# Kernel tuning notes

Hardware: AMD Instinct MI355X
Metric: run time of the kernel (lower is better)

Reference implementation:

```python
import jax, jax.numpy as jnp
import numpy as np

B, C, H = 16, 512, 32
HID, NB, S, P, SR = 512, 36, 26, 7, 2
SCALE = 32.0
N_LOC, N_LOC_LAB = 12, 8
N_GRP, GRP_SZ, N_GRP_LAB = 4, 6, 16
IN_DIM = P * P * C


def roi_align(feat, coords, scale, pooled, sr):
    # feat: (B,C,H,W); coords: (B,NB,4) normalized xyxy. torchvision roi_align,
    # aligned=False, fixed sampling_ratio=sr (adaptive ratio is data-dependent).
    Bs, Cc, Hh, Ww = feat.shape
    x1 = coords[..., 0] * scale
    y1 = coords[..., 1] * scale
    x2 = coords[..., 2] * scale
    y2 = coords[..., 3] * scale
    rw = jnp.maximum(x2 - x1, 1.0)
    rh = jnp.maximum(y2 - y1, 1.0)
    bw = rw / pooled
    bh = rh / pooled
    # sample offsets within roi, in bin units: (pooled*sr,)
    off = (jnp.arange(pooled)[:, None] + (jnp.arange(sr) + 0.5) / sr).reshape(-1)
    ys = y1[..., None] + off * bh[..., None]  # (B,NB,pooled*sr)
    xs = x1[..., None] + off * bw[..., None]

    def prep(t, size):
        valid = (t > -1.0) & (t < size)
        tc = jnp.clip(t, 0.0, size - 1)
        lo = jnp.floor(tc).astype(jnp.int32)
        hi = jnp.minimum(lo + 1, size - 1)
        frac = tc - lo
        return lo, hi, frac, valid

    y_lo, y_hi, ly, vy = prep(ys, Hh)
    x_lo, x_hi, lx, vx = prep(xs, Ww)
    hy, hx = 1.0 - ly, 1.0 - lx

    featl = feat.transpose(0, 2, 3, 1)  # (B,H,W,C)
    b_idx = jnp.arange(Bs)[:, None, None, None]

    def gather(yi, xi):
        # -> (B,NB,Py,Px,C)
        return featl[b_idx, yi[:, :, :, None], xi[:, :, None, :]]

    def w(a, b):
        return (a[..., :, None] * b[..., None, :])[..., None]

    val = (gather(y_lo, x_lo) * w(hy, hx) + gather(y_lo, x_hi) * w(hy, lx)
           + gather(y_hi, x_lo) * w(ly, hx) + gather(y_hi, x_hi) * w(ly, lx))
    mask = (vy[:, :, :, None] & vx[:, :, None, :])[..., None]
    val = jnp.where(mask, val, 0.0)
    val = val.reshape(Bs, -1, pooled, sr, pooled, sr, Cc).mean(axis=(3, 5))
    return val.transpose(0, 1, 4, 2, 3)  # (B,NB,C,pooled,pooled)


def setup_inputs() -> dict:
    key = jax.random.key(0)
    ks = jax.random.split(key, 10)
    lf = jax.random.normal(ks[0], (B, C, H, H), dtype=jnp.float32)
    xs = jnp.sort(jax.random.uniform(ks[1], (B, S, 2)), axis=-1)
    ys = jnp.sort(jax.random.uniform(ks[2], (B, S, 2)), axis=-1)
    coords = jnp.stack([xs[..., 0], ys[..., 0], xs[..., 1], ys[..., 1]], axis=-1)
    sc = 0.02
    return {
        'local_features': lf,
        'pred_bbox_coords': coords,
        'roi_fc_W': jax.random.normal(ks[3], (HID, IN_DIM), dtype=jnp.float32) * sc,
        'roi_fc_b': jnp.zeros((HID,), jnp.float32),
        'coords_W': jax.random.normal(ks[4], (S, 4, HID), dtype=jnp.float32) * sc,
        'coords_b': jnp.zeros((S, 4), jnp.float32),
        'pres_W': jax.random.normal(ks[5], (S, HID), dtype=jnp.float32) * sc,
        'pres_b': jnp.zeros((S,), jnp.float32),
        'loc_W': jax.random.normal(ks[6], (N_LOC, N_LOC_LAB, HID), dtype=jnp.float32) * sc,
        'loc_b': jnp.zeros((N_LOC, N_LOC_LAB), jnp.float32),
        'grp_W': jax.random.normal(ks[7], (N_GRP, N_GRP_LAB, GRP_SZ * HID), dtype=jnp.float32) * sc,
        'grp_b': jnp.zeros((N_GRP, N_GRP_LAB), jnp.float32),
        'loc_idx': jnp.arange(N_LOC, dtype=jnp.int32),
        'grp_idx': jnp.arange(N_GRP * GRP_SZ, dtype=jnp.int32).reshape(N_GRP, GRP_SZ),
    }


def reference(local_features, pred_bbox_coords, roi_fc_W, roi_fc_b, coords_W,
              coords_b, pres_W, pres_b, loc_W, loc_b, grp_W, grp_b, loc_idx, grp_idx):
    Bs = local_features.shape[0]
    # boxes S..NB default to the full image (0,0,1,1)
    full = jnp.broadcast_to(jnp.array([0.0, 0.0, 1.0, 1.0], jnp.float32), (Bs, NB, 4))
    coords_all = full.at[:, :S].set(pred_bbox_coords)
    roi = roi_align(local_features, coords_all, SCALE, P, SR)  # (B,NB,C,P,P)
    flat = roi.reshape(Bs, NB, IN_DIM)
    feats = jax.nn.relu(jnp.einsum('bnf,hf->bnh', flat, roi_fc_W) + roi_fc_b)
    sup = feats[:, :S]  # (B,S,HID)
    # per-box coord refinement heads
    deltas = jnp.einsum('bsh,soh->bso', sup, coords_W) + coords_b  # (B,S,4)
    w = pred_bbox_coords[..., 2] - pred_bbox_coords[..., 0]
    h = pred_bbox_coords[..., 3] - pred_bbox_coords[..., 1]
    wh = jnp.stack([w, h, w, h], axis=-1)
    refined = pred_bbox_coords + deltas * wh
    presence = jnp.einsum('bsh,sh->bs', sup, pres_W) + pres_b  # (B,S)
    # per-box MLC heads
    loc = jnp.einsum('blh,loh->blo', feats[:, loc_idx], loc_W) + loc_b
    # per-group MLC heads (concat box feats within group along hidden)
    gf = feats[:, grp_idx].reshape(Bs, N_GRP, GRP_SZ * HID)
    grp = jnp.einsum('bgk,gok->bgo', gf, grp_W) + grp_b
    mlc = jnp.concatenate([loc.reshape(Bs, -1), grp.reshape(Bs, -1)], axis=1)
    return refined, presence, mlc
```

## Files before the change

### kernel.cpp

```cpp
#include <hip/hip_runtime.h>

typedef unsigned short u16;
typedef __attribute__((ext_vector_type(8))) short short8;
typedef __attribute__((ext_vector_type(8))) unsigned short ushort8_t;
typedef __attribute__((ext_vector_type(4))) float f32x4;
typedef __attribute__((ext_vector_type(2))) float v2f;

#define BATCH   16
#define CCH     512
#define NBOX    36
#define SS      26
#define INDIM   25088
#define HIDN    512
#define M_ROWS  576
#define KSPLIT  28
#define KITERS  14

__device__ __forceinline__ u16 f2bf(float f) {
  unsigned u = __float_as_uint(f);
  u += 0x7FFF + ((u >> 16) & 1);
  return (u16)(u >> 16);
}
__device__ __forceinline__ float bf2f(u16 h) {
  return __uint_as_float(((unsigned)h) << 16);
}
__device__ __forceinline__ v2f bf2x2(u16 a, u16 b) {
  v2f r;
  r.x = __uint_as_float(((unsigned)a) << 16);
  r.y = __uint_as_float(((unsigned)b) << 16);
  return r;
}

typedef __attribute__((address_space(3))) void* as3_ptr;
typedef const __attribute__((address_space(1))) void* as1_cptr;
__device__ __forceinline__ void gload_lds16(const void* g, void* l) {
  __builtin_amdgcn_global_load_lds((as1_cptr)g, (as3_ptr)l, 16, 0, 0);
}

__global__ __launch_bounds__(256) void k_transpose_lf(const float* __restrict__ in,
                                                      u16* __restrict__ out) {
  __shared__ float t[32][33];
  int b = blockIdx.z, ct = blockIdx.y, pt = blockIdx.x;
  int tx = threadIdx.x, ty = threadIdx.y;
#pragma unroll
  for (int i = 0; i < 4; ++i) {
    int c = ct * 32 + ty + i * 8;
    int p = pt * 32 + tx;
    t[ty + i * 8][tx] = in[((size_t)b * CCH + c) * 1024 + p];
  }
  __syncthreads();
#pragma unroll
  for (int i = 0; i < 4; ++i) {
    int p = pt * 32 + ty + i * 8;
    int c = ct * 32 + tx;
    out[((size_t)b * 1024 + p) * CCH + c] = f2bf(t[tx][ty + i * 8]);
  }
}

__global__ __launch_bounds__(256) void k_convert_w(const float4* __restrict__ in,
                                                   ushort4* __restrict__ out) {
  int i = blockIdx.x * 256 + threadIdx.x;
  float4 v = in[i];
  ushort4 o;
  o.x = f2bf(v.x); o.y = f2bf(v.y); o.z = f2bf(v.z); o.w = f2bf(v.w);
  out[i] = o;
}

__global__ __launch_bounds__(512) void k_roi(const u16* __restrict__ lf_t,
                                             const float* __restrict__ pred,
                                             u16* __restrict__ flat) {
  __shared__ int   s_ylo[14], s_yhi[14], s_xlo[14], s_xhi[14];
  __shared__ float s_wyl[14], s_wyh[14], s_wxl[14], s_wxh[14];
  __shared__ u16   s_out[INDIM];

  int blk = blockIdx.x;
  int b = blk / NBOX, n = blk % NBOX;
  int t = threadIdx.x;

  if (t < 28) {
    bool isY = t < 14;
    int j = isY ? t : t - 14;
    float c0, c1, c2, c3;
    if (n < SS) {
      const float* p = pred + ((size_t)(b * SS + n)) * 4;
      c0 = p[0]; c1 = p[1]; c2 = p[2]; c3 = p[3];
    } else { c0 = 0.f; c1 = 0.f; c2 = 1.f; c3 = 1.f; }
    float lo1 = (isY ? c1 : c0) * 32.f;
    float hi1 = (isY ? c3 : c2) * 32.f;
    float sz = fmaxf(hi1 - lo1, 1.f);
    float bs = sz * (1.f / 7.f);
    float off = (float)(j >> 1) + 0.25f + 0.5f * (float)(j & 1);
    float pos = lo1 + off * bs;
    bool valid = (pos > -1.f) && (pos < 32.f);
    float tc = fminf(fmaxf(pos, 0.f), 31.f);
    int lo = (int)floorf(tc);
    int hi = min(lo + 1, 31);
    float fr = tc - (float)lo;
    float wl = valid ? (1.f - fr) : 0.f;
    float wh = valid ? fr : 0.f;
    if (isY) { s_ylo[j] = lo; s_yhi[j] = hi; s_wyl[j] = wl; s_wyh[j] = wh; }
    else     { s_xlo[j] = lo; s_xhi[j] = hi; s_wxl[j] = wl; s_wxh[j] = wh; }
  }
  __syncthreads();

  int cg = t & 63;
  int pg = t >> 6;
  const u16* base = lf_t + (size_t)b * 1024 * CCH + cg * 8;

  for (int p = pg; p < 49; p += 8) {
    int py = p / 7, px = p % 7;
    v2f a0 = {0.f, 0.f}, a1 = {0.f, 0.f}, a2 = {0.f, 0.f}, a3 = {0.f, 0.f};
#pragma unroll
    for (int sy = 0; sy < 2; ++sy) {
      int jy = 2 * py + sy;
      const u16* rlo = base + s_ylo[jy] * 32 * CCH;
      const u16* rhi = base + s_yhi[jy] * 32 * CCH;
      float wyl = s_wyl[jy], wyh = s_wyh[jy];
#pragma unroll
      for (int sx = 0; sx < 2; ++sx) {
        int jx = 2 * px + sx;
        int xl = s_xlo[jx] * CCH, xh = s_xhi[jx] * CCH;
        v2f wll = {wyl * s_wxl[jx], wyl * s_wxl[jx]};
        v2f wlh = {wyl * s_wxh[jx], wyl * s_wxh[jx]};
        v2f whl = {wyh * s_wxl[jx], wyh * s_wxl[jx]};
        v2f whh = {wyh * s_wxh[jx], wyh * s_wxh[jx]};
        ushort8_t vll = *(const ushort8_t*)(rlo + xl);
        ushort8_t vlh = *(const ushort8_t*)(rlo + xh);
        ushort8_t vhl = *(const ushort8_t*)(rhi + xl);
        ushort8_t vhh = *(const ushort8_t*)(rhi + xh);
        a0 += wll * bf2x2(vll[0], vll[1]) + wlh * bf2x2(vlh[0], vlh[1])
            + whl * bf2x2(vhl[0], vhl[1]) + whh * bf2x2(vhh[0], vhh[1]);
        a1 += wll * bf2x2(vll[2], vll[3]) + wlh * bf2x2(vlh[2], vlh[3])
            + whl * bf2x2(vhl[2], vhl[3]) + whh * bf2x2(vhh[2], vhh[3]);
        a2 += wll * bf2x2(vll[4], vll[5]) + wlh * bf2x2(vlh[4], vlh[5])
            + whl * bf2x2(vhl[4], vhl[5]) + whh * bf2x2(vhh[4], vhh[5]);
        a3 += wll * bf2x2(vll[6], vll[7]) + wlh * bf2x2(vlh[6], vlh[7])
            + whl * bf2x2(vhl[6], vhl[7]) + whh * bf2x2(vhh[6], vhh[7]);
      }
    }
    int c0i = cg * 8;
    s_out[(c0i + 0) * 49 + p] = f2bf(a0.x * 0.25f);
    s_out[(c0i + 1) * 49 + p] = f2bf(a0.y * 0.25f);
    s_out[(c0i + 2) * 49 + p] = f2bf(a1.x * 0.25f);
    s_out[(c0i + 3) * 49 + p] = f2bf(a1.y * 0.25f);
    s_out[(c0i + 4) * 49 + p] = f2bf(a2.x * 0.25f);
    s_out[(c0i + 5) * 49 + p] = f2bf(a2.y * 0.25f);
    s_out[(c0i + 6) * 49 + p] = f2bf(a3.x * 0.25f);
    s_out[(c0i + 7) * 49 + p] = f2bf(a3.y * 0.25f);
  }
  __syncthreads();

  uint4* dst = (uint4*)(flat + (size_t)blk * INDIM);
  const uint4* src = (const uint4*)s_out;
  for (int i = t; i < INDIM / 8; i += 512) dst[i] = src[i];
}

__global__ __launch_bounds__(256) void k_gemm(const u16* __restrict__ flat,
                                              const u16* __restrict__ Wb,
                                              float* __restrict__ partials) {
  __shared__ u16 As[128 * 64];
  __shared__ u16 Bs[64 * 64];

  int tid = threadIdx.x;
  int wave = tid >> 6, lane = tid & 63;
  int wm = wave >> 1, wn = wave & 1;
  int quad = lane >> 4, r = lane & 15;
  int xb = r & 7;

  int tileM0 = blockIdx.y * 128;
  int tileN0 = blockIdx.x * 64;
  int kbase = blockIdx.z * (KITERS * 64);

  f32x4 acc[4][2];
#pragma unroll
  for (int mi = 0; mi < 4; ++mi)
#pragma unroll
    for (int ni = 0; ni < 2; ++ni) acc[mi][ni] = (f32x4){0.f, 0.f, 0.f, 0.f};

  for (int kt = 0; kt < KITERS; ++kt) {
    int k0 = kbase + kt * 64;
#pragma unroll
    for (int t = 0; t < 4; ++t) {
      int chunk = (wave * 4 + t) * 64 + lane;
      int row = chunk >> 3;
      int pcol = chunk & 7;
      int lcol = ((pcol ^ (row & 7)) << 3);
      int grow = min(tileM0 + row, M_ROWS - 1);
      gload_lds16(flat + (size_t)grow * INDIM + k0 + lcol,
                  &As[(wave * 4 + t) * 512]);
    }
#pragma unroll
    for (int t = 0; t < 2; ++t) {
      int chunk = (wave * 2 + t) * 64 + lane;
      int row = chunk >> 3;
      int pcol = chunk & 7;
      int lcol = ((pcol ^ (row & 7)) << 3);
      int nrow = tileN0 + row;
      gload_lds16(Wb + (size_t)nrow * INDIM + k0 + lcol,
                  &Bs[(wave * 2 + t) * 512]);
    }
    __syncthreads();

#pragma unroll
    for (int kk = 0; kk < 64; kk += 32) {
      int k8 = kk >> 3;
      int pc = ((k8 + quad) ^ xb) << 3;
      short8 af[4], bfr[2];
#pragma unroll
      for (int mi = 0; mi < 4; ++mi)
        af[mi] = *(const short8*)&As[(wm * 64 + mi * 16 + r) * 64 + pc];
#pragma unroll
      for (int ni = 0; ni < 2; ++ni)
        bfr[ni] = *(const short8*)&Bs[(wn * 32 + ni * 16 + r) * 64 + pc];
#pragma unroll
      for (int mi = 0; mi < 4; ++mi)
#pragma unroll
        for (int ni = 0; ni < 2; ++ni)
          acc[mi][ni] = __builtin_amdgcn_mfma_f32_16x16x32_bf16(
              af[mi], bfr[ni], acc[mi][ni], 0, 0, 0);
    }
    __syncthreads();
  }

  float* part = partials + (size_t)blockIdx.z * (M_ROWS * HIDN);
#pragma unroll
  for (int mi = 0; mi < 4; ++mi)
#pragma unroll
    for (int ni = 0; ni < 2; ++ni) {
      int row0 = tileM0 + wm * 64 + mi * 16 + quad * 4;
      int col = tileN0 + wn * 32 + ni * 16 + r;
#pragma unroll
      for (int reg = 0; reg < 4; ++reg) {
        int row = row0 + reg;
        if (row < M_ROWS) part[(size_t)row * HIDN + col] = acc[mi][ni][reg];
      }
    }
}

__global__ __launch_bounds__(256) void k_reduce(const float* __restrict__ partials,
                                                const float* __restrict__ bias,
                                                float* __restrict__ feats) {
  int gid = blockIdx.x * 256 + threadIdx.x;
  int h = gid & (HIDN - 1);
  float s = 0.f;
#pragma unroll
  for (int k = 0; k < KSPLIT; ++k) s += partials[(size_t)k * (M_ROWS * HIDN) + gid];
  s += bias[h];
  feats[gid] = fmaxf(s, 0.f);
}

__device__ __forceinline__ float wave_red(float s) {
#pragma unroll
  for (int off = 32; off > 0; off >>= 1) s += __shfl_down(s, off);
  return s;
}

__device__ __forceinline__ float dot512(const float* __restrict__ f,
                                        const float* __restrict__ w, int lane) {
  const float4* f4 = (const float4*)f;
  const float4* w4 = (const float4*)w;
  float4 x0 = f4[lane], y0 = w4[lane];
  float4 x1 = f4[lane + 64], y1 = w4[lane + 64];
  return x0.x * y0.x + x0.y * y0.y + x0.z * y0.z + x0.w * y0.w +
         x1.x * y1.x + x1.y * y1.y + x1.z * y1.z + x1.w * y1.w;
}

__global__ __launch_bounds__(256) void k_heads(const float* __restrict__ feats,
                                               const float* __restrict__ pred,
                                               const float* __restrict__ cW,
                                               const float* __restrict__ cb,
                                               const float* __restrict__ pW,
                                               const float* __restrict__ pb,
                                               const float* __restrict__ lW,
                                               const float* __restrict__ lb,
                                               const float* __restrict__ gW,
                                               const float* __restrict__ gb,
                                               const int* __restrict__ lidx,
                                               const int* __restrict__ gidx,
                                               float* __restrict__ out) {
  int wid = blockIdx.x * 4 + (threadIdx.x >> 6);
  int lane = threadIdx.x & 63;
  float sum = 0.f;

  if (wid < 1664) {
    int b = wid / 104, rr = wid % 104, s = rr >> 2, o = rr & 3;
    sum = dot512(feats + (size_t)(b * NBOX + s) * HIDN,
                 cW + (size_t)(s * 4 + o) * HIDN, lane);
    sum = wave_red(sum);
    if (lane == 0) {
      const float* p = pred + (size_t)(b * SS + s) * 4;
      float wdt = p[2] - p[0], hgt = p[3] - p[1];
      float whv = (o & 1) ? hgt : wdt;
      out[wid] = p[o] + (sum + cb[s * 4 + o]) * whv;
    }
  } else if (wid < 2080) {
    int i = wid - 1664;
    int b = i / 26, s = i % 26;
    sum = dot512(feats + (size_t)(b * NBOX + s) * HIDN,
                 pW + (size_t)s * HIDN, lane);
    sum = wave_red(sum);
    if (lane == 0) out[1664 + i] = sum + pb[s];
  } else if (wid < 3616) {
    int i = wid - 2080;
    int b = i / 96, rr = i % 96, l = rr >> 3, o = rr & 7;
    sum = dot512(feats + (size_t)(b * NBOX + lidx[l]) * HIDN,
                 lW + (size_t)(l * 8 + o) * HIDN, lane);
    sum = wave_red(sum);
    if (lane == 0) out[2080 + b * 160 + rr] = sum + lb[l * 8 + o];
  } else {
    int i = wid - 3616;
    int b = i / 64, rr = i % 64, g = rr >> 4, o = rr & 15;
    const float* w = gW + (size_t)(g * 16 + o) * 3072;
#pragma unroll
    for (int jj = 0; jj < 6; ++jj) {
      sum += dot512(feats + (size_t)(b * NBOX + gidx[g * 6 + jj]) * HIDN,
                    w + jj * 512, lane);
    }
    sum = wave_red(sum);
    if (lane == 0) out[2080 + b * 160 + 96 + rr] = sum + gb[g * 16 + o];
  }
}

extern "C" void kernel_launch(void* const* d_in, const int* in_sizes, int n_in,
                              void* d_out, int out_size, void* d_ws, size_t ws_size,
                              hipStream_t stream) {
  const float* lf      = (const float*)d_in[0];
  const float* pred    = (const float*)d_in[1];
  const float* roiW    = (const float*)d_in[2];
  const float* roiB    = (const float*)d_in[3];
  const float* cW      = (const float*)d_in[4];
  const float* cb      = (const float*)d_in[5];
  const float* pW      = (const float*)d_in[6];
  const float* pb      = (const float*)d_in[7];
  const float* lW      = (const float*)d_in[8];
  const float* lb      = (const float*)d_in[9];
  const float* gW      = (const float*)d_in[10];
  const float* gb      = (const float*)d_in[11];
  const int*   lidx    = (const int*)d_in[12];
  const int*   gidx    = (const int*)d_in[13];
  float* out = (float*)d_out;

  char* ws = (char*)d_ws;
  u16*   lf_t     = (u16*)ws;
  float* partials = (float*)ws;
  u16*   Wb   = (u16*)(ws + 33030144);
  u16*   flat = (u16*)(ws + 33030144 + 25690112);
  float* feats = (float*)(ws + 33030144 + 25690112 + 28901376);

  k_transpose_lf<<<dim3(32, 16, 16), dim3(32, 8), 0, stream>>>(lf, lf_t);
  k_convert_w<<<12544, 256, 0, stream>>>((const float4*)roiW, (ushort4*)Wb);
  k_roi<<<576, 512, 0, stream>>>(lf_t, pred, flat);
  k_gemm<<<dim3(8, 5, KSPLIT), 256, 0, stream>>>(flat, Wb, partials);
  k_reduce<<<(M_ROWS * HIDN) / 256, 256, 0, stream>>>(partials, roiB, feats);
  k_heads<<<1160, 256, 0, stream>>>(feats, pred, cW, cb, pW, pb, lW, lb, gW, gb,
                                    lidx, gidx, out);
}
```

Measured before the change: 225.2 us.

## Widen GEMM tile to 128x128 with register prefetch, vectorize transpose and reduce

The GEMM tile grows from 128x64 to 128x128, and the direct global-to-LDS loads are replaced by register-staged prefetch of the next K slice, so global loads overlap with the MFMA work. The feature transpose now reads float4 and writes 8-wide bf16 vectors per thread, and the split-K reduction uses float4 loads. The larger tile halves the number of GEMM blocks (4x5x28) and raises register pressure, which may lower occupancy.

```diff
diff --git a/kernel.cpp b/kernel.cpp
--- a/kernel.cpp
+++ b/kernel.cpp
@@ -31,30 +31,29 @@
   return r;
 }
 
-typedef __attribute__((address_space(3))) void* as3_ptr;
-typedef const __attribute__((address_space(1))) void* as1_cptr;
-__device__ __forceinline__ void gload_lds16(const void* g, void* l) {
-  __builtin_amdgcn_global_load_lds((as1_cptr)g, (as3_ptr)l, 16, 0, 0);
-}
-
 __global__ __launch_bounds__(256) void k_transpose_lf(const float* __restrict__ in,
                                                       u16* __restrict__ out) {
-  __shared__ float t[32][33];
-  int b = blockIdx.z, ct = blockIdx.y, pt = blockIdx.x;
-  int tx = threadIdx.x, ty = threadIdx.y;
-#pragma unroll
-  for (int i = 0; i < 4; ++i) {
-    int c = ct * 32 + ty + i * 8;
-    int p = pt * 32 + tx;
-    t[ty + i * 8][tx] = in[((size_t)b * CCH + c) * 1024 + p];
-  }
+  __shared__ u16 t[32][66];
+  int b = blockIdx.z, y = blockIdx.y, ct = blockIdx.x;
+  int tid = threadIdx.x;
+
+  int cl = tid >> 2;
+  int xq = (tid & 3) * 8;
+  const float* src = in + ((size_t)(b * CCH + ct * 64 + cl) * 1024) + y * 32 + xq;
+  float4 v0 = *(const float4*)src;
+  float4 v1 = *(const float4*)(src + 4);
+  t[xq + 0][cl] = f2bf(v0.x); t[xq + 1][cl] = f2bf(v0.y);
+  t[xq + 2][cl] = f2bf(v0.z); t[xq + 3][cl] = f2bf(v0.w);
+  t[xq + 4][cl] = f2bf(v1.x); t[xq + 5][cl] = f2bf(v1.y);
+  t[xq + 6][cl] = f2bf(v1.z); t[xq + 7][cl] = f2bf(v1.w);
   __syncthreads();
-#pragma unroll
-  for (int i = 0; i < 4; ++i) {
-    int p = pt * 32 + ty + i * 8;
-    int c = ct * 32 + tx;
-    out[((size_t)b * 1024 + p) * CCH + c] = f2bf(t[tx][ty + i * 8]);
-  }
+
+  int xl = tid >> 3;
+  int cq = (tid & 7) * 8;
+  ushort8_t o;
+#pragma unroll
+  for (int i = 0; i < 8; ++i) o[i] = t[xl][cq + i];
+  *(ushort8_t*)(out + ((size_t)b * 1024 + y * 32 + xl) * CCH + ct * 64 + cq) = o;
 }
 
 __global__ __launch_bounds__(256) void k_convert_w(const float4* __restrict__ in,
@@ -159,7 +158,7 @@
                                               const u16* __restrict__ Wb,
                                               float* __restrict__ partials) {
   __shared__ u16 As[128 * 64];
-  __shared__ u16 Bs[64 * 64];
+  __shared__ u16 Bs[128 * 64];
 
   int tid = threadIdx.x;
   int wave = tid >> 6, lane = tid & 63;
@@ -168,54 +167,67 @@
   int xb = r & 7;
 
   int tileM0 = blockIdx.y * 128;
-  int tileN0 = blockIdx.x * 64;
+  int tileN0 = blockIdx.x * 128;
   int kbase = blockIdx.z * (KITERS * 64);
 
-  f32x4 acc[4][2];
+  size_t aoff[4], boff[4];
+  int    ldso[4];
+#pragma unroll
+  for (int t = 0; t < 4; ++t) {
+    int chunk = (wave * 4 + t) * 64 + lane;
+    int row = chunk >> 3;
+    int lc = chunk & 7;
+    ldso[t] = row * 64 + ((lc ^ (row & 7)) << 3);
+    int grow = min(tileM0 + row, M_ROWS - 1);
+    aoff[t] = (size_t)grow * INDIM + kbase + lc * 8;
+    boff[t] = (size_t)(tileN0 + row) * INDIM + kbase + lc * 8;
+  }
+
+  f32x4 acc[4][4];
 #pragma unroll
   for (int mi = 0; mi < 4; ++mi)
 #pragma unroll
-    for (int ni = 0; ni < 2; ++ni) acc[mi][ni] = (f32x4){0.f, 0.f, 0.f, 0.f};
+    for (int ni = 0; ni < 4; ++ni) acc[mi][ni] = (f32x4){0.f, 0.f, 0.f, 0.f};
+
+  short8 ra[4], rb[4];
+#pragma unroll
+  for (int t = 0; t < 4; ++t) {
+    ra[t] = *(const short8*)(flat + aoff[t]);
+    rb[t] = *(const short8*)(Wb + boff[t]);
+  }
 
   for (int kt = 0; kt < KITERS; ++kt) {
-    int k0 = kbase + kt * 64;
 #pragma unroll
     for (int t = 0; t < 4; ++t) {
-      int chunk = (wave * 4 + t) * 64 + lane;
-      int row = chunk >> 3;
-      int pcol = chunk & 7;
-      int lcol = ((pcol ^ (row & 7)) << 3);
-      int grow = min(tileM0 + row, M_ROWS - 1);
-      gload_lds16(flat + (size_t)grow * INDIM + k0 + lcol,
-                  &As[(wave * 4 + t) * 512]);
-    }
-#pragma unroll
-    for (int t = 0; t < 2; ++t) {
-      int chunk = (wave * 2 + t) * 64 + lane;
-      int row = chunk >> 3;
-      int pcol = chunk & 7;
-      int lcol = ((pcol ^ (row & 7)) << 3);
-      int nrow = tileN0 + row;
-      gload_lds16(Wb + (size_t)nrow * INDIM + k0 + lcol,
-                  &Bs[(wave * 2 + t) * 512]);
+      *(short8*)&As[ldso[t]] = ra[t];
+      *(short8*)&Bs[ldso[t]] = rb[t];
     }
     __syncthreads();
+
+    if (kt + 1 < KITERS) {
+      int kadv = (kt + 1) * 64;
+#pragma unroll
+      for (int t = 0; t < 4; ++t) {
+        ra[t] = *(const short8*)(flat + aoff[t] + kadv);
+        rb[t] = *(const short8*)(Wb + boff[t] + kadv);
+      }
+    }
 
 #pragma unroll
     for (int kk = 0; kk < 64; kk += 32) {
       int k8 = kk >> 3;
       int pc = ((k8 + quad) ^ xb) << 3;
-      short8 af[4], bfr[2];
+      short8 af[4], bfr[4];
 #pragma unroll
       for (int mi = 0; mi < 4; ++mi)
         af[mi] = *(const short8*)&As[(wm * 64 + mi * 16 + r) * 64 + pc];
 #pragma unroll
-      for (int ni = 0; ni < 2; ++ni)
-        bfr[ni] = *(const short8*)&Bs[(wn * 32 + ni * 16 + r) * 64 + pc];
+      for (int ni = 0; ni < 4; ++ni)
+        bfr[ni] = *(const short8*)&Bs[(wn * 64 + ni * 16 + r) * 64 + pc];
 #pragma unroll
       for (int mi = 0; mi < 4; ++mi)
 #pragma unroll
-        for (int ni = 0; ni < 2; ++ni)
+        for (int ni = 0; ni < 4; ++ni)
           acc[mi][ni] = __builtin_amdgcn_mfma_f32_16x16x32_bf16(
               af[mi], bfr[ni], acc[mi][ni], 0, 0, 0);
     }
@@ -226,9 +238,9 @@
 #pragma unroll
   for (int mi = 0; mi < 4; ++mi)
 #pragma unroll
-    for (int ni = 0; ni < 2; ++ni) {
+    for (int ni = 0; ni < 4; ++ni) {
       int row0 = tileM0 + wm * 64 + mi * 16 + quad * 4;
-      int col = tileN0 + wn * 32 + ni * 16 + r;
+      int col = tileN0 + wn * 64 + ni * 16 + r;
 #pragma unroll
       for (int reg = 0; reg < 4; ++reg) {
         int row = row0 + reg;
@@ -237,16 +249,23 @@
     }
 }
 
-__global__ __launch_bounds__(256) void k_reduce(const float* __restrict__ partials,
+__global__ __launch_bounds__(256) void k_reduce(const float4* __restrict__ partials,
                                                 const float* __restrict__ bias,
-                                                float* __restrict__ feats) {
+                                                float4* __restrict__ feats) {
   int gid = blockIdx.x * 256 + threadIdx.x;
-  int h = gid & (HIDN - 1);
-  float s = 0.f;
-#pragma unroll
-  for (int k = 0; k < KSPLIT; ++k) s += partials[(size_t)k * (M_ROWS * HIDN) + gid];
-  s += bias[h];
-  feats[gid] = fmaxf(s, 0.f);
+  int h4 = gid & (HIDN / 4 - 1);
+  float4 s = {0.f, 0.f, 0.f, 0.f};
+#pragma unroll
+  for (int k = 0; k < KSPLIT; ++k) {
+    float4 v = partials[(size_t)k * (M_ROWS * HIDN / 4) + gid];
+    s.x += v.x; s.y += v.y; s.z += v.z; s.w += v.w;
+  }
+  const float* bi = bias + h4 * 4;
+  s.x = fmaxf(s.x + bi[0], 0.f);
+  s.y = fmaxf(s.y + bi[1], 0.f);
+  s.z = fmaxf(s.z + bi[2], 0.f);
+  s.w = fmaxf(s.w + bi[3], 0.f);
+  feats[gid] = s;
 }
 
 __device__ __forceinline__ float wave_red(float s) {
@@ -347,11 +366,12 @@
   u16*   flat = (u16*)(ws + 33030144 + 25690112);
   float* feats = (float*)(ws + 33030144 + 25690112 + 28901376);
 
-  k_transpose_lf<<<dim3(32, 16, 16), dim3(32, 8), 0, stream>>>(lf, lf_t);
+  k_transpose_lf<<<dim3(8, 32, 16), 256, 0, stream>>>(lf, lf_t);
   k_convert_w<<<12544, 256, 0, stream>>>((const float4*)roiW, (ushort4*)Wb);
   k_roi<<<576, 512, 0, stream>>>(lf_t, pred, flat);
-  k_gemm<<<dim3(8, 5, KSPLIT), 256, 0, stream>>>(flat, Wb, partials);
-  k_reduce<<<(M_ROWS * HIDN) / 256, 256, 0, stream>>>(partials, roiB, feats);
+  k_gemm<<<dim3(4, 5, KSPLIT), 256, 0, stream>>>(flat, Wb, partials);
+  k_reduce<<<(M_ROWS * HIDN / 4) / 256, 256, 0, stream>>>(
+      (const float4*)partials, roiB, (float4*)feats);
   k_heads<<<1160, 256, 0, stream>>>(feats, pred, cW, cb, pW, pb, lW, lb, gW, gb,
                                     lidx, gidx, out);
 }
```

Result: no change. 221.0 us (-1.9%).
